# Kernel tuning notes

Measured on AMD Instinct MI355X. Metric: run time of the kernel, lower is better.

The kernel has to match this reference:

```python
import jax, jax.numpy as jnp
import numpy as np

INF = 1000000000.0
N_HEAD, QK, VD, NVAR = 4, 4, 4, 1


def _rope(xh, tf, thetas):
    # xh: [B, L, H, D], tf: [B, L], thetas: [D//2]
    freqs = tf[:, :, None] * thetas                     # [B, L, D//2]
    cos = jnp.cos(freqs)[:, :, None, :]                 # broadcast over heads
    sin = jnp.sin(freqs)[:, :, None, :]
    xr, xi = xh[..., 0::2], xh[..., 1::2]               # complex pairs
    out_r = xr * cos - xi * sin
    out_i = xr * sin + xi * cos
    return jnp.stack([out_r, out_i], axis=-1).reshape(xh.shape)


def setup_inputs() -> dict:
    key = jax.random.key(0)
    ks = jax.random.split(key, 11)
    bn, pn, pl = 32, 64, 128
    s = 0.1
    return {
        "x": jax.random.normal(ks[0], (bn, pn, pl), jnp.float32),
        "t": jax.random.uniform(ks[1], (bn, pn, pl), jnp.float32),
        "mask": jax.random.randint(ks[2], (bn, pn, pl), 0, 2, jnp.int32),
        "Wq": jax.random.normal(ks[3], (N_HEAD * QK, NVAR), jnp.float32) * s,
        "Wk": jax.random.normal(ks[4], (N_HEAD * QK, NVAR), jnp.float32) * s,
        "Wv": jax.random.normal(ks[5], (N_HEAD * VD, NVAR), jnp.float32) * s,
        "Wout": jax.random.normal(ks[6], (NVAR, N_HEAD * VD), jnp.float32) * s,
        "W1": jax.random.normal(ks[7], (4 * N_HEAD * VD, N_HEAD * VD), jnp.float32) * s,
        "b1": jnp.zeros((4 * N_HEAD * VD,), jnp.float32),
        "W2": jax.random.normal(ks[8], (N_HEAD * VD, 4 * N_HEAD * VD), jnp.float32) * s,
        "b2": jnp.zeros((N_HEAD * VD,), jnp.float32),
    }


def reference(x, t, mask, Wq, Wk, Wv, Wout, W1, b1, W2, b2):
    bn, pn, pl = x.shape
    B = bn * pn
    thetas = 1.0 / (1000.0 ** (jnp.arange(0, QK, 2, dtype=jnp.float32) / QK))
    x4 = x[..., None]                                       # [bn, pn, pl, 1]
    q = jnp.einsum('bpln,dn->bpld', x4, Wq).reshape(B, pl, N_HEAD, QK)
    k = jnp.einsum('bpln,dn->bpld', x4, Wk).reshape(B, pl, N_HEAD, QK)
    v = jnp.einsum('bpln,dn->bpld', x4, Wv).reshape(B, pl, N_HEAD, VD)
    tf = t.reshape(B, pl)
    q = _rope(q, tf, thetas)
    k = _rope(k, tf, thetas)
    q = q.transpose(0, 2, 1, 3)                             # [B, H, L, D]
    k = k.transpose(0, 2, 1, 3)
    v = v.transpose(0, 2, 1, 3)
    scale = QK ** 0.5
    attn = jnp.einsum('bhqd,bhkd->bhqk', q / scale, k)      # [B, H, L, L]
    m = mask.reshape(B, pl)
    mask_mat = (m[:, :, None] * m[:, None, :])[:, None, :, :]
    attn = jnp.where(mask_mat == 0, -INF, attn)
    attn = jax.nn.softmax(attn, axis=-1)
    o = jnp.einsum('bhqk,bhkd->bhqd', attn, v)
    o = o.transpose(0, 2, 1, 3).reshape(bn, pn, pl, N_HEAD * VD)
    ffn = jnp.maximum(o @ W1.T + b1, 0.0) @ W2.T + b2       # dropout off (eval)
    out_q = o + ffn
    return out_q @ Wout.T                                   # [bn, pn, pl, 1]
```

## Files before the change

### kernel.cpp

```cpp
#include <hip/hip_runtime.h>

constexpr int PL = 128;

typedef float f32x2 __attribute__((ext_vector_type(2)));

__device__ __forceinline__ float fast_exp2(float x) {
#if __has_builtin(__builtin_amdgcn_exp2f)
    return __builtin_amdgcn_exp2f(x);
#else
    return __expf(x * 0.69314718055994531f);
#endif
}
__device__ __forceinline__ f32x2 pk_fma(f32x2 a, f32x2 b, f32x2 c) {
    return __builtin_elementwise_fma(a, b, c);
}
__device__ __forceinline__ f32x2 sp(float v) { f32x2 r; r.x = v; r.y = v; return r; }

__global__ __launch_bounds__(256, 4) void fused_block_kernel(
    const float* __restrict__ x, const float* __restrict__ t, const int* __restrict__ mask,
    const float* __restrict__ Wq, const float* __restrict__ Wk, const float* __restrict__ Wv,
    const float* __restrict__ Wout, const float* __restrict__ W1, const float* __restrict__ b1,
    const float* __restrict__ W2, const float* __restrict__ b2,
    float* __restrict__ out)
{
    __shared__ float4 CSMc[2][64 * 3];
    __shared__ float4 ROWD[2][PL];
    __shared__ float  validR[2][PL];
    __shared__ f32x2  w1p[32][16];
    __shared__ __align__(8) float cg[64];
    __shared__ __align__(8) float b1s[64];
    __shared__ float  OST[2][4][PL];
    __shared__ float  xpart[2][2];
    __shared__ int    wcnt[2][2];
    __shared__ __align__(16) float woutS[16];
    __shared__ float  bbS;

    const int tid  = threadIdx.x;
    const int blk  = blockIdx.x;
    const int seq  = tid >> 7;
    const int j    = tid & 127;
    const int lane = tid & 63;
    const int wh   = (tid >> 6) & 1;

    const float xv = x[(blk * 2 + seq) * PL + j];
    const float tv = t[(blk * 2 + seq) * PL + j];
    const int   mv = mask[(blk * 2 + seq) * PL + j];
    const float va = mv ? 1.0f : 0.0f;
    float xc0v, xs0v, xc1v, xs1v;
    {
        const float th1 = 0.031622776601683794f;
        xc0v = xv * __cosf(tv);        xs0v = xv * __sinf(tv);
        xc1v = xv * __cosf(tv * th1);  xs1v = xv * __sinf(tv * th1);
        ROWD[seq][j]   = make_float4(xc0v, xs0v, xc1v, xs1v);
        validR[seq][j] = va;
        float px = xv;
        #pragma unroll
        for (int off = 32; off >= 1; off >>= 1) px += __shfl_xor(px, off);
        if (lane == 0) xpart[seq][wh] = px;
    }
    const unsigned long long ball = __ballot(mv != 0);
    const int lpos = __popcll(ball & ((1ull << lane) - 1ull));
    if (lane == 0) wcnt[seq][wh] = __popcll(ball);

    #pragma unroll
    for (int k = 0; k < 4; ++k) {
        const int idx = tid + k * 256;
        const int hid = idx >> 4, d = idx & 15;
        reinterpret_cast<float*>(w1p)[((hid >> 1) * 16 + d) * 2 + (hid & 1)] = W1[idx];
    }
    if (tid < 64) {
        b1s[tid] = b1[tid];
        float c = 0.f;
        #pragma unroll
        for (int d = 0; d < 16; ++d) c += W2[d * 64 + tid] * Wout[d];
        cg[tid] = c;
    }
    if (tid < 16) woutS[tid] = Wout[tid];
    if (tid == 0) {
        float bb = 0.f;
        #pragma unroll
        for (int d = 0; d < 16; ++d) bb += b2[d] * Wout[d];
        bbS = bb;
    }
    __syncthreads();

    {
        float* C = reinterpret_cast<float*>(CSMc[seq]);
        const int pos = lpos + (wh ? wcnt[seq][0] : 0);
        if (mv) {
            const int p = pos >> 1, par = pos & 1;
            C[p*12 + 0 + par] = xc0v;
            C[p*12 + 2 + par] = xs0v;
            C[p*12 + 4 + par] = xc1v;
            C[p*12 + 6 + par] = xs1v;
            C[p*12 + 8 + par] = 1.0f;
            C[p*12 +10 + par] = xv;
        }
        const int nv = wcnt[seq][0] + wcnt[seq][1];
        if (j == 0 && (nv & 1)) {
            const int p = nv >> 1;
            C[p*12 + 1] = 0.f; C[p*12 + 3] = 0.f; C[p*12 + 5] = 0.f;
            C[p*12 + 7] = 0.f; C[p*12 + 9] = 0.f; C[p*12 +11] = 0.f;
        }
    }
    __syncthreads();

    {
        const int wave = tid >> 6;
        const int sq   = wave >> 1;
        const int hh   = wave & 1;
        const int l2   = tid & 63;
        const int h    = hh * 2 + (l2 >> 5);
        const int r0   = l2 & 31;
        const float4 wq4 = reinterpret_cast<const float4*>(Wq)[h];
        const float4 wk4 = reinterpret_cast<const float4*>(Wk)[h];
        const float a0  = wq4.x*wk4.x + wq4.y*wk4.y;
        const float be0 = wq4.x*wk4.y - wq4.y*wk4.x;
        const float a1  = wq4.z*wk4.z + wq4.w*wk4.w;
        const float be1 = wq4.z*wk4.w - wq4.w*wk4.z;
        const float gam = 0.5f * 1.4426950408889634f;

        float vr[4];
        f32x2 A[4], Bc[4], Cc[4], Dc[4], S[4], X[4];
        #pragma unroll
        for (int rr = 0; rr < 4; ++rr) {
            const int r = r0 + rr * 32;
            const float4 rd = ROWD[sq][r];
            vr[rr] = validR[sq][r];
            A[rr]  = sp(gam * (rd.x * a0 + rd.y * be0));
            Bc[rr] = sp(gam * (rd.y * a0 - rd.x * be0));
            Cc[rr] = sp(gam * (rd.z * a1 + rd.w * be1));
            Dc[rr] = sp(gam * (rd.w * a1 - rd.z * be1));
            S[rr] = sp(0.f);
            X[rr] = sp(0.f);
        }
        const int nv    = wcnt[sq][0] + wcnt[sq][1];
        const int npair = (nv + 1) >> 1;
        #pragma unroll 2
        for (int jj = 0; jj < npair; ++jj) {
            const float4 ca = CSMc[sq][jj * 3 + 0];
            const float4 cb = CSMc[sq][jj * 3 + 1];
            const float4 mm = CSMc[sq][jj * 3 + 2];
            f32x2 c0p; c0p.x = ca.x; c0p.y = ca.y;
            f32x2 s0p; s0p.x = ca.z; s0p.y = ca.w;
            f32x2 c1p; c1p.x = cb.x; c1p.y = cb.y;
            f32x2 s1p; s1p.x = cb.z; s1p.y = cb.w;
            f32x2 vv;  vv.x  = mm.x; vv.y  = mm.y;
            f32x2 vx;  vx.x  = mm.z; vx.y  = mm.w;
            #pragma unroll
            for (int rr = 0; rr < 4; ++rr) {
                f32x2 L = A[rr] * c0p;
                L = pk_fma(Bc[rr], s0p, L);
                L = pk_fma(Cc[rr], c1p, L);
                L = pk_fma(Dc[rr], s1p, L);
                f32x2 E;
                E.x = fast_exp2(L.x);
                E.y = fast_exp2(L.y);
                S[rr] = pk_fma(E, vv, S[rr]);
                X[rr] = pk_fma(E, vx, X[rr]);
            }
        }
        const float sumx = xpart[sq][0] + xpart[sq][1];
        #pragma unroll
        for (int rr = 0; rr < 4; ++rr) {
            const int r = r0 + rr * 32;
            const float s  = S[rr].x + S[rr].y;
            const float wx = X[rr].x + X[rr].y;
            const bool  m  = vr[rr] != 0.f;
            OST[sq][h][r] = (m ? wx : sumx) / (m ? s : 128.f);
        }
    }
    __syncthreads();

    {
        const int qi = j;
        const float vmask = validR[seq][qi];
        (void)vmask;
        const float os0 = OST[seq][0][qi], os1 = OST[seq][1][qi];
        const float os2 = OST[seq][2][qi], os3 = OST[seq][3][qi];
        const float4 wv0 = reinterpret_cast<const float4*>(Wv)[0];
        const float4 wv1 = reinterpret_cast<const float4*>(Wv)[1];
        const float4 wv2 = reinterpret_cast<const float4*>(Wv)[2];
        const float4 wv3 = reinterpret_cast<const float4*>(Wv)[3];
        float o[16];
        o[ 0] = wv0.x*os0; o[ 1] = wv0.y*os0; o[ 2] = wv0.z*os0; o[ 3] = wv0.w*os0;
        o[ 4] = wv1.x*os1; o[ 5] = wv1.y*os1; o[ 6] = wv1.z*os1; o[ 7] = wv1.w*os1;
        o[ 8] = wv2.x*os2; o[ 9] = wv2.y*os2; o[10] = wv2.z*os2; o[11] = wv2.w*os2;
        o[12] = wv3.x*os3; o[13] = wv3.y*os3; o[14] = wv3.z*os3; o[15] = wv3.w*os3;

        const f32x2* b1pair = reinterpret_cast<const f32x2*>(b1s);
        const f32x2* cgpair = reinterpret_cast<const f32x2*>(cg);
        f32x2 R2 = sp(0.f);
        #pragma unroll 4
        for (int p = 0; p < 32; ++p) {
            f32x2 HS = b1pair[p];
            #pragma unroll
            for (int d = 0; d < 16; ++d) HS = pk_fma(w1p[p][d], sp(o[d]), HS);
            HS.x = fmaxf(HS.x, 0.f);
            HS.y = fmaxf(HS.y, 0.f);
            R2 = pk_fma(cgpair[p], HS, R2);
        }
        float r = R2.x + R2.y + bbS;
        #pragma unroll
        for (int d = 0; d < 16; ++d) r += o[d] * woutS[d];
        out[(blk * 2 + seq) * PL + qi] = r;
    }
}

extern "C" void kernel_launch(void* const* d_in, const int* in_sizes, int n_in,
                              void* d_out, int out_size, void* d_ws, size_t ws_size,
                              hipStream_t stream) {
    const float* x    = (const float*)d_in[0];
    const float* t    = (const float*)d_in[1];
    const int*   mask = (const int*)d_in[2];
    const float* Wq   = (const float*)d_in[3];
    const float* Wk   = (const float*)d_in[4];
    const float* Wv   = (const float*)d_in[5];
    const float* Wout = (const float*)d_in[6];
    const float* W1   = (const float*)d_in[7];
    const float* b1   = (const float*)d_in[8];
    const float* W2   = (const float*)d_in[9];
    const float* b2   = (const float*)d_in[10];
    float* outp = (float*)d_out;
    const int B  = in_sizes[0] / PL;
    const int B2 = B / 2;
    fused_block_kernel<<<B2, 256, 0, stream>>>(x, t, mask, Wq, Wk, Wv, Wout, W1, b1, W2, b2, outp);
}
```

Baseline: 27.14 us.

## Compact query rows to valid positions and skip masked-query attention work

Builds a shared-memory list of valid (unmasked) row indices and computes attention only for those query rows. A templated core is specialised by the number of 32-row slots needed. Masked query rows get the uniform mean of x in the FFN stage instead. With about half the mask set, this should roughly halve the exp work in the attention loop. The cost is a runtime switch over template instantiations and an indirect ROWD load.

```diff
diff --git a/kernel.cpp b/kernel.cpp
--- a/kernel.cpp
+++ b/kernel.cpp
@@ -15,6 +15,65 @@
     return __builtin_elementwise_fma(a, b, c);
 }
 __device__ __forceinline__ f32x2 sp(float v) { f32x2 r; r.x = v; r.y = v; return r; }
+
+template <int NS>
+__device__ __forceinline__ void attn_core(
+    const float4* __restrict__ CSMc_s, const int* __restrict__ rowList_s,
+    const float4* __restrict__ ROWD_s, float* __restrict__ OST_h,
+    int npair, int nv, int r0,
+    float a0, float be0, float a1, float be1)
+{
+    const float gam = 0.5f * 1.4426950408889634f;
+    f32x2 A[NS], Bc[NS], Cc[NS], Dc[NS], S[NS], X[NS];
+    int  rowv[NS];
+    bool act[NS];
+    #pragma unroll
+    for (int rr = 0; rr < NS; ++rr) {
+        const int i = r0 + rr * 32;
+        act[rr]  = (i < nv);
+        const int row = act[rr] ? rowList_s[i] : 0;
+        rowv[rr] = row;
+        const float4 rd = ROWD_s[row];
+        A[rr]  = sp(gam * (rd.x * a0 + rd.y * be0));
+        Bc[rr] = sp(gam * (rd.y * a0 - rd.x * be0));
+        Cc[rr] = sp(gam * (rd.z * a1 + rd.w * be1));
+        Dc[rr] = sp(gam * (rd.w * a1 - rd.z * be1));
+        S[rr]  = sp(0.f);
+        X[rr]  = sp(0.f);
+    }
+    #pragma unroll 2
+    for (int jj = 0; jj < npair; ++jj) {
+        const float4 ca = CSMc_s[jj * 3 + 0];
+        const float4 cb = CSMc_s[jj * 3 + 1];
+        const float4 mm = CSMc_s[jj * 3 + 2];
+        f32x2 c0p; c0p.x = ca.x; c0p.y = ca.y;
+        f32x2 s0p; s0p.x = ca.z; s0p.y = ca.w;
+        f32x2 c1p; c1p.x = cb.x; c1p.y = cb.y;
+        f32x2 s1p; s1p.x = cb.z; s1p.y = cb.w;
+        f32x2 vv;  vv.x  = mm.x; vv.y  = mm.y;
+        f32x2 vx;  vx.x  = mm.z; vx.y  = mm.w;
+        #pragma unroll
+        for (int rr = 0; rr < NS; ++rr) {
+            f32x2 L = A[rr] * c0p;
+            L = pk_fma(Bc[rr], s0p, L);
+            L = pk_fma(Cc[rr], c1p, L);
+            L = pk_fma(Dc[rr], s1p, L);
+            f32x2 E;
+            E.x = fast_exp2(L.x);
+            E.y = fast_exp2(L.y);
+            S[rr] = pk_fma(E, vv, S[rr]);
+            X[rr] = pk_fma(E, vx, X[rr]);
+        }
+    }
+    #pragma unroll
+    for (int rr = 0; rr < NS; ++rr) {
+        if (act[rr]) {
+            const float s  = S[rr].x + S[rr].y;
+            const float wx = X[rr].x + X[rr].y;
+            OST_h[rowv[rr]] = wx / s;
+        }
+    }
+}
 
 __global__ __launch_bounds__(256, 4) void fused_block_kernel(
     const float* __restrict__ x, const float* __restrict__ t, const int* __restrict__ mask,
@@ -26,6 +85,7 @@
     __shared__ float4 CSMc[2][64 * 3];
     __shared__ float4 ROWD[2][PL];
     __shared__ float  validR[2][PL];
+    __shared__ int    rowList[2][PL];
     __shared__ f32x2  w1p[32][16];
     __shared__ __align__(8) float cg[64];
     __shared__ __align__(8) float b1s[64];
@@ -95,6 +155,7 @@
             C[p*12 + 6 + par] = xs1v;
             C[p*12 + 8 + par] = 1.0f;
             C[p*12 +10 + par] = xv;
+            rowList[seq][pos] = j;
         }
         const int nv = wcnt[seq][0] + wcnt[seq][1];
         if (j == 0 && (nv & 1)) {
@@ -118,66 +179,32 @@
         const float be0 = wq4.x*wk4.y - wq4.y*wk4.x;
         const float a1  = wq4.z*wk4.z + wq4.w*wk4.w;
         const float be1 = wq4.z*wk4.w - wq4.w*wk4.z;
-        const float gam = 0.5f * 1.4426950408889634f;
-
-        float vr[4];
-        f32x2 A[4], Bc[4], Cc[4], Dc[4], S[4], X[4];
-        #pragma unroll
-        for (int rr = 0; rr < 4; ++rr) {
-            const int r = r0 + rr * 32;
-            const float4 rd = ROWD[sq][r];
-            vr[rr] = validR[sq][r];
-            A[rr]  = sp(gam * (rd.x * a0 + rd.y * be0));
-            Bc[rr] = sp(gam * (rd.y * a0 - rd.x * be0));
-            Cc[rr] = sp(gam * (rd.z * a1 + rd.w * be1));
-            Dc[rr] = sp(gam * (rd.w * a1 - rd.z * be1));
-            S[rr] = sp(0.f);
-            X[rr] = sp(0.f);
-        }
+
         const int nv    = wcnt[sq][0] + wcnt[sq][1];
         const int npair = (nv + 1) >> 1;
-        #pragma unroll 2
-        for (int jj = 0; jj < npair; ++jj) {
-            const float4 ca = CSMc[sq][jj * 3 + 0];
-            const float4 cb = CSMc[sq][jj * 3 + 1];
-            const float4 mm = CSMc[sq][jj * 3 + 2];
-            f32x2 c0p; c0p.x = ca.x; c0p.y = ca.y;
-            f32x2 s0p; s0p.x = ca.z; s0p.y = ca.w;
-            f32x2 c1p; c1p.x = cb.x; c1p.y = cb.y;
-            f32x2 s1p; s1p.x = cb.z; s1p.y = cb.w;
-            f32x2 vv;  vv.x  = mm.x; vv.y  = mm.y;
-            f32x2 vx;  vx.x  = mm.z; vx.y  = mm.w;
-            #pragma unroll
-            for (int rr = 0; rr < 4; ++rr) {
-                f32x2 L = A[rr] * c0p;
-                L = pk_fma(Bc[rr], s0p, L);
-                L = pk_fma(Cc[rr], c1p, L);
-                L = pk_fma(Dc[rr], s1p, L);
-                f32x2 E;
-                E.x = fast_exp2(L.x);
-                E.y = fast_exp2(L.y);
-                S[rr] = pk_fma(E, vv, S[rr]);
-                X[rr] = pk_fma(E, vx, X[rr]);
-            }
-        }
-        const float sumx = xpart[sq][0] + xpart[sq][1];
-        #pragma unroll
-        for (int rr = 0; rr < 4; ++rr) {
-            const int r = r0 + rr * 32;
-            const float s  = S[rr].x + S[rr].y;
-            const float wx = X[rr].x + X[rr].y;
-            const bool  m  = vr[rr] != 0.f;
-            OST[sq][h][r] = (m ? wx : sumx) / (m ? s : 128.f);
+        const int nslot = (nv + 31) >> 5;
+        const float4* Cs = CSMc[sq];
+        const int*    rl = rowList[sq];
+        const float4* rd = ROWD[sq];
+        float*        oh = &OST[sq][h][0];
+        switch (nslot) {
+            case 0: break;
+            case 1: attn_core<1>(Cs, rl, rd, oh, npair, nv, r0, a0, be0, a1, be1); break;
+            case 2: attn_core<2>(Cs, rl, rd, oh, npair, nv, r0, a0, be0, a1, be1); break;
+            case 3: attn_core<3>(Cs, rl, rd, oh, npair, nv, r0, a0, be0, a1, be1); break;
+            default: attn_core<4>(Cs, rl, rd, oh, npair, nv, r0, a0, be0, a1, be1); break;
         }
     }
     __syncthreads();
 
     {
         const int qi = j;
-        const float vmask = validR[seq][qi];
-        (void)vmask;
-        const float os0 = OST[seq][0][qi], os1 = OST[seq][1][qi];
-        const float os2 = OST[seq][2][qi], os3 = OST[seq][3][qi];
+        const bool mq = validR[seq][qi] != 0.f;
+        const float sm = (xpart[seq][0] + xpart[seq][1]) * (1.0f / 128.0f);
+        const float os0 = mq ? OST[seq][0][qi] : sm;
+        const float os1 = mq ? OST[seq][1][qi] : sm;
+        const float os2 = mq ? OST[seq][2][qi] : sm;
+        const float os3 = mq ? OST[seq][3][qi] : sm;
         const float4 wv0 = reinterpret_cast<const float4*>(Wv)[0];
         const float4 wv1 = reinterpret_cast<const float4*>(Wv)[1];
         const float4 wv2 = reinterpret_cast<const float4*>(Wv)[2];
```

Result: slower. 28.86 us (+6.3%).
